# Optimization experiments

Hardware: AMD Instinct MI355X
Metric: run time of the kernel (lower is better)

The kernel has to match this reference:

```python
import jax, jax.numpy as jnp
import numpy as np

MAX_CHILD = 64  # max trie branching factor (padding width for per-row child windows)


def setup_inputs() -> dict:
    key = jax.random.key(0)
    B, D, V, N = 1024, 1024, 32000, 200000
    k1, k2, k3, k4 = jax.random.split(key, 4)
    x = jax.random.normal(k1, (B, D), dtype=jnp.float32)
    weight = jax.random.normal(k2, (V, D), dtype=jnp.float32) * 0.02
    bias = jax.random.normal(k3, (V,), dtype=jnp.float32) * 0.02
    # Build a consistent CompactCSRTrie: offsets [N+1], tokens/child_nodes [E]
    rng = np.random.default_rng(0)
    deg = rng.integers(1, MAX_CHILD + 1, size=N)
    offsets = np.zeros(N + 1, dtype=np.int32)
    offsets[1:] = np.cumsum(deg)
    E = int(offsets[-1])
    tokens = rng.integers(0, V, size=E).astype(np.int32)
    child_nodes = rng.integers(0, N, size=E).astype(np.int32)
    cur_node = jax.random.randint(k4, (B,), 0, N, dtype=jnp.int32)
    return {
        "x": x,
        "weight": weight,
        "bias": bias,
        "cur_node": cur_node,
        "offsets": jnp.asarray(offsets),
        "tokens": jnp.asarray(tokens),
        "child_nodes": jnp.asarray(child_nodes),
        "step": 1,
    }


def reference(x, weight, bias, cur_node, offsets, tokens, child_nodes, step):
    # Dense GEMM part of the fused kernel: logits = x @ W^T + b  -> [B, V]
    logits = jnp.einsum("bd,vd->bv", x, weight) + bias
    B, V = logits.shape

    # CSR trie traversal: per row, the children of cur_node are
    # tokens[offsets[cur]:offsets[cur+1]] (valid next tokens) and
    # child_nodes[...] (next trie nodes). Gather a padded MAX_CHILD window.
    start = offsets[cur_node]                              # [B]
    deg = offsets[cur_node + 1] - start                    # [B]
    pos = jnp.arange(MAX_CHILD, dtype=start.dtype)         # [C]
    idx = jnp.minimum(start[:, None] + pos[None, :], tokens.shape[0] - 1)  # [B, C]
    valid = pos[None, :] < deg[:, None]                    # [B, C] bool

    tok = tokens[idx]                                      # [B, C] valid token columns
    child = child_nodes[idx]                               # [B, C] next trie nodes

    # Validity masking: only valid child tokens keep their logit, rest -> -inf
    rows = jnp.arange(B)[:, None]
    mask = jnp.zeros((B, V), dtype=bool).at[rows, tok].max(valid)
    masked_logits = jnp.where(mask, logits, -jnp.inf)

    next_nodes = jnp.where(valid, child, -1)               # [B, C], -1 padded
    valid_idxs = jnp.where(valid, tok, -1)                 # [B, C], -1 padded
    return next_nodes, valid_idxs, masked_logits
```

## Files before the change

kernel.cpp:

```cpp
#include <hip/hip_runtime.h>
#include <math.h>

#define B_ 1024
#define D_ 1024
#define V_ 32000
#define MAXC 64
#define BLOCK 1024

#define NEG_FILL (-3.0e38f)

typedef float vfloat4 __attribute__((ext_vector_type(4)));

__global__ __launch_bounds__(BLOCK) void constrained_linear_kernel(
    const float* __restrict__ x,
    const float* __restrict__ weight,
    const float* __restrict__ bias,
    const int* __restrict__ cur_node,
    const int* __restrict__ offsets,
    const int* __restrict__ tokens,
    const int* __restrict__ child_nodes,
    float* __restrict__ next_nodes,
    float* __restrict__ valid_idxs,
    float* __restrict__ masked_logits)
{
    __shared__ float xs[D_];
    const int b = blockIdx.x;
    const int tid = threadIdx.x;

    const float4* x4 = reinterpret_cast<const float4*>(x + (size_t)b * D_);
    float4* xs4 = reinterpret_cast<float4*>(xs);
    if (tid < D_ / 4) xs4[tid] = x4[tid];

    const int cur = cur_node[b];
    const int start = offsets[cur];
    int deg = offsets[cur + 1] - start;
    if (deg > MAXC) deg = MAXC;

    float* ml_row = masked_logits + (size_t)b * V_;
    vfloat4* ml4 = reinterpret_cast<vfloat4*>(ml_row);
    const vfloat4 fill4 = {NEG_FILL, NEG_FILL, NEG_FILL, NEG_FILL};
    #pragma unroll 2
    for (int i = tid; i < V_ / 4; i += BLOCK)
        __builtin_nontemporal_store(fill4, &ml4[i]);

    if (tid < MAXC) {
        float nn = -1.0f, vi = -1.0f;
        if (tid < deg) {
            const int e = start + tid;
            nn = (float)child_nodes[e];
            vi = (float)tokens[e];
        }
        next_nodes[b * MAXC + tid] = nn;
        valid_idxs[b * MAXC + tid] = vi;
    }

    __syncthreads();

    const int wave = tid >> 6;
    const int lane = tid & 63;

    for (int c = wave; c < deg; c += BLOCK / 64) {
        const int tok = tokens[start + c];
        const float4* w4 = reinterpret_cast<const float4*>(weight + (size_t)tok * D_);
        float acc = 0.0f;
        #pragma unroll
        for (int k = 0; k < 4; ++k) {
            const float4 wv = w4[k * 64 + lane];
            const float4 xv = xs4[k * 64 + lane];
            acc += wv.x * xv.x + wv.y * xv.y + wv.z * xv.z + wv.w * xv.w;
        }
        #pragma unroll
        for (int off = 32; off > 0; off >>= 1)
            acc += __shfl_xor(acc, off);
        if (lane == 0)
            __builtin_nontemporal_store(acc + bias[tok], &ml_row[tok]);
    }
}

extern "C" void kernel_launch(void* const* d_in, const int* in_sizes, int n_in,
                              void* d_out, int out_size, void* d_ws, size_t ws_size,
                              hipStream_t stream) {
    const float* x           = (const float*)d_in[0];
    const float* weight      = (const float*)d_in[1];
    const float* bias        = (const float*)d_in[2];
    const int*   cur_node    = (const int*)d_in[3];
    const int*   offsets     = (const int*)d_in[4];
    const int*   tokens      = (const int*)d_in[5];
    const int*   child_nodes = (const int*)d_in[6];

    float* out = (float*)d_out;
    float* next_nodes    = out;
    float* valid_idxs    = out + (size_t)B_ * MAXC;
    float* masked_logits = out + 2 * (size_t)B_ * MAXC;

    constrained_linear_kernel<<<B_, BLOCK, 0, stream>>>(
        x, weight, bias, cur_node, offsets, tokens, child_nodes,
        next_nodes, valid_idxs, masked_logits);
}
```

Baseline: 48.93 us.

## Split into separate fill kernel and per-child wave-parallel gather kernel

Replaces the single per-row kernel with two launches. A grid-stride fill kernel writes the -1 padding and the -inf sentinel over the whole output, and a gather kernel gives each (row, child) pair its own wave to compute the dot product and scatter the logit. This removes the per-row barrier and the uneven work across rows, and spreads the 131 MB fill over a flat grid. In exchange it adds a second launch, rewrites the padded slots twice, and reads x from global memory instead of shared memory.

Measured after the change: 63.90 us. 1.31x slower.

```diff
diff --git a/kernel.cpp b/kernel.cpp
--- a/kernel.cpp
+++ b/kernel.cpp
@@ -5,13 +5,30 @@
 #define D_ 1024
 #define V_ 32000
 #define MAXC 64
-#define BLOCK 1024
 
 #define NEG_FILL (-3.0e38f)
 
 typedef float vfloat4 __attribute__((ext_vector_type(4)));
 
-__global__ __launch_bounds__(BLOCK) void constrained_linear_kernel(
+#define FILL_BLOCKS 2048
+#define FILL_TPB 256
+#define NV4 ((2 * B_ * MAXC) / 4)
+#define TOT4 ((2 * B_ * MAXC + B_ * V_) / 4)
+
+__global__ __launch_bounds__(FILL_TPB) void fill_kernel(float* __restrict__ out)
+{
+    vfloat4* o4 = reinterpret_cast<vfloat4*>(out);
+    const vfloat4 neg1 = {-1.0f, -1.0f, -1.0f, -1.0f};
+    const vfloat4 sent = {NEG_FILL, NEG_FILL, NEG_FILL, NEG_FILL};
+    for (int i = blockIdx.x * FILL_TPB + threadIdx.x; i < TOT4;
+         i += FILL_BLOCKS * FILL_TPB) {
+        __builtin_nontemporal_store(i < NV4 ? neg1 : sent, &o4[i]);
+    }
+}
+
+#define G_TPB 1024
+
+__global__ __launch_bounds__(G_TPB) void gather_kernel(
     const float* __restrict__ x,
     const float* __restrict__ weight,
     const float* __restrict__ bias,
@@ -23,58 +40,37 @@
     float* __restrict__ valid_idxs,
     float* __restrict__ masked_logits)
 {
-    __shared__ float xs[D_];
-    const int b = blockIdx.x;
-    const int tid = threadIdx.x;
-
-    const float4* x4 = reinterpret_cast<const float4*>(x + (size_t)b * D_);
-    float4* xs4 = reinterpret_cast<float4*>(xs);
-    if (tid < D_ / 4) xs4[tid] = x4[tid];
+    const int gw = blockIdx.x * (G_TPB / 64) + (threadIdx.x >> 6);
+    const int lane = threadIdx.x & 63;
+    const int b = gw >> 6;
+    const int c = gw & (MAXC - 1);
 
     const int cur = cur_node[b];
     const int start = offsets[cur];
-    int deg = offsets[cur + 1] - start;
-    if (deg > MAXC) deg = MAXC;
+    const int deg = offsets[cur + 1] - start;
+    if (c >= deg) return;
 
-    float* ml_row = masked_logits + (size_t)b * V_;
-    vfloat4* ml4 = reinterpret_cast<vfloat4*>(ml_row);
-    const vfloat4 fill4 = {NEG_FILL, NEG_FILL, NEG_FILL, NEG_FILL};
-    #pragma unroll 2
-    for (int i = tid; i < V_ / 4; i += BLOCK)
-        __builtin_nontemporal_store(fill4, &ml4[i]);
+    const int e = start + c;
+    const int tok = tokens[e];
 
-    if (tid < MAXC) {
-        float nn = -1.0f, vi = -1.0f;
-        if (tid < deg) {
-            const int e = start + tid;
-            nn = (float)child_nodes[e];
-            vi = (float)tokens[e];
-        }
-        next_nodes[b * MAXC + tid] = nn;
-        valid_idxs[b * MAXC + tid] = vi;
+    if (lane == 0) valid_idxs[b * MAXC + c] = (float)tok;
+    if (lane == 1) next_nodes[b * MAXC + c] = (float)child_nodes[e];
+
+    const float4* w4 = reinterpret_cast<const float4*>(weight + (size_t)tok * D_);
+    const float4* x4 = reinterpret_cast<const float4*>(x + (size_t)b * D_);
+    float acc = 0.0f;
+    #pragma unroll
+    for (int k = 0; k < 4; ++k) {
+        const float4 wv = w4[k * 64 + lane];
+        const float4 xv = x4[k * 64 + lane];
+        acc += wv.x * xv.x + wv.y * xv.y + wv.z * xv.z + wv.w * xv.w;
     }
+    #pragma unroll
+    for (int off = 32; off > 0; off >>= 1)
+        acc += __shfl_xor(acc, off);
 
-    __syncthreads();
-
-    const int wave = tid >> 6;
-    const int lane = tid & 63;
-
-    for (int c = wave; c < deg; c += BLOCK / 64) {
-        const int tok = tokens[start + c];
-        const float4* w4 = reinterpret_cast<const float4*>(weight + (size_t)tok * D_);
-        float acc = 0.0f;
-        #pragma unroll
-        for (int k = 0; k < 4; ++k) {
-            const float4 wv = w4[k * 64 + lane];
-            const float4 xv = xs4[k * 64 + lane];
-            acc += wv.x * xv.x + wv.y * xv.y + wv.z * xv.z + wv.w * xv.w;
-        }
-        #pragma unroll
-        for (int off = 32; off > 0; off >>= 1)
-            acc += __shfl_xor(acc, off);
-        if (lane == 0)
-            __builtin_nontemporal_store(acc + bias[tok], &ml_row[tok]);
-    }
+    if (lane == 0)
+        masked_logits[(size_t)b * V_ + tok] = acc + bias[tok];
 }
 
 extern "C" void kernel_launch(void* const* d_in, const int* in_sizes, int n_in,
@@ -93,7 +89,8 @@
     float* valid_idxs    = out + (size_t)B_ * MAXC;
     float* masked_logits = out + 2 * (size_t)B_ * MAXC;
 
-    constrained_linear_kernel<<<B_, BLOCK, 0, stream>>>(
+    fill_kernel<<<FILL_BLOCKS, FILL_TPB, 0, stream>>>(out);
+    gather_kernel<<<(B_ * MAXC) / (G_TPB / 64), G_TPB, 0, stream>>>(
         x, weight, bias, cur_node, offsets, tokens, child_nodes,
         next_nodes, valid_idxs, masked_logits);
 }
```

## Prefetch weight rows into registers before fill stores and drop shared x staging

Applied to the files above, without the earlier changes.

Each wave now loads its x slice and all of its up-to-four assigned weight rows into registers before the fill loop, so the gather latency overlaps the -inf fill stores of the logit row. The dot products are computed before the barrier, and only the final scalar writes happen after it. Shared memory staging of x is removed, and launch bounds request 4 waves per SIMD. The cost is much higher register pressure (64 float4 weight values per lane), which may cap occupancy or cause spills.

Result: faster. 47.73 us (-2.5%).

```diff
diff --git a/kernel.cpp b/kernel.cpp
--- a/kernel.cpp
+++ b/kernel.cpp
@@ -11,7 +11,7 @@
 
 typedef float vfloat4 __attribute__((ext_vector_type(4)));
 
-__global__ __launch_bounds__(BLOCK) void constrained_linear_kernel(
+__global__ __launch_bounds__(BLOCK, 4) void constrained_linear_kernel(
     const float* __restrict__ x,
     const float* __restrict__ weight,
     const float* __restrict__ bias,
@@ -23,25 +23,39 @@
     float* __restrict__ valid_idxs,
     float* __restrict__ masked_logits)
 {
-    __shared__ float xs[D_];
     const int b = blockIdx.x;
     const int tid = threadIdx.x;
-
-    const float4* x4 = reinterpret_cast<const float4*>(x + (size_t)b * D_);
-    float4* xs4 = reinterpret_cast<float4*>(xs);
-    if (tid < D_ / 4) xs4[tid] = x4[tid];
+    const int wave = tid >> 6;
+    const int lane = tid & 63;
 
     const int cur = cur_node[b];
     const int start = offsets[cur];
     int deg = offsets[cur + 1] - start;
     if (deg > MAXC) deg = MAXC;
 
-    float* ml_row = masked_logits + (size_t)b * V_;
-    vfloat4* ml4 = reinterpret_cast<vfloat4*>(ml_row);
-    const vfloat4 fill4 = {NEG_FILL, NEG_FILL, NEG_FILL, NEG_FILL};
-    #pragma unroll 2
-    for (int i = tid; i < V_ / 4; i += BLOCK)
-        __builtin_nontemporal_store(fill4, &ml4[i]);
+    const float4* x4 = reinterpret_cast<const float4*>(x + (size_t)b * D_);
+    float4 xv[4];
+    #pragma unroll
+    for (int k = 0; k < 4; ++k)
+        xv[k] = x4[k * 64 + lane];
+
+    float4 wv[4][4];
+    float bj[4];
+    int   tk[4];
+    #pragma unroll
+    for (int j = 0; j < 4; ++j) {
+        const int c = wave + 16 * j;
+        if (c < deg) {
+            const int e = start + c;
+            const int t = tokens[e];
+            tk[j] = t;
+            bj[j] = bias[t];
+            const float4* w4 = reinterpret_cast<const float4*>(weight + (size_t)t * D_);
+            #pragma unroll
+            for (int k = 0; k < 4; ++k)
+                wv[j][k] = w4[k * 64 + lane];
+        }
+    }
 
     if (tid < MAXC) {
         float nn = -1.0f, vi = -1.0f;
@@ -54,26 +68,37 @@
         valid_idxs[b * MAXC + tid] = vi;
     }
 
+    float* ml_row = masked_logits + (size_t)b * V_;
+    vfloat4* ml4 = reinterpret_cast<vfloat4*>(ml_row);
+    const vfloat4 sent = {NEG_FILL, NEG_FILL, NEG_FILL, NEG_FILL};
+    #pragma unroll 2
+    for (int i = tid; i < V_ / 4; i += BLOCK)
+        __builtin_nontemporal_store(sent, &ml4[i]);
+
+    float accs[4];
+    #pragma unroll
+    for (int j = 0; j < 4; ++j) {
+        const int c = wave + 16 * j;
+        if (c < deg) {
+            float acc = 0.0f;
+            #pragma unroll
+            for (int k = 0; k < 4; ++k)
+                acc += wv[j][k].x * xv[k].x + wv[j][k].y * xv[k].y +
+                       wv[j][k].z * xv[k].z + wv[j][k].w * xv[k].w;
+            #pragma unroll
+            for (int off = 32; off > 0; off >>= 1)
+                acc += __shfl_xor(acc, off);
+            accs[j] = acc + bj[j];
+        }
+    }
+
     __syncthreads();
 
-    const int wave = tid >> 6;
-    const int lane = tid & 63;
-
-    for (int c = wave; c < deg; c += BLOCK / 64) {
-        const int tok = tokens[start + c];
-        const float4* w4 = reinterpret_cast<const float4*>(weight + (size_t)tok * D_);
-        float acc = 0.0f;
-        #pragma unroll
-        for (int k = 0; k < 4; ++k) {
-            const float4 wv = w4[k * 64 + lane];
-            const float4 xv = xs4[k * 64 + lane];
-            acc += wv.x * xv.x + wv.y * xv.y + wv.z * xv.z + wv.w * xv.w;
-        }
-        #pragma unroll
-        for (int off = 32; off > 0; off >>= 1)
-            acc += __shfl_xor(acc, off);
-        if (lane == 0)
-            __builtin_nontemporal_store(acc + bias[tok], &ml_row[tok]);
+    #pragma unroll
+    for (int j = 0; j < 4; ++j) {
+        const int c = wave + 16 * j;
+        if (c < deg && lane == 0)
+            ml_row[tk[j]] = accs[j];
     }
 }
 
```

## Split each row across sixteen vocab-slice blocks with slice-local dot products

Applied to the files above, without the earlier changes.

The grid becomes 16 blocks of 256 threads per batch row instead of one 1024-thread block. Each block fills only its 2000-token slice of the masked logits row with the sentinel and computes dot products only for child tokens that fall in that slice. Winning values are staged in shared memory and written after a barrier, which orders them after the fill in the same block and drops the cross-block fill race. x is now read straight from global memory rather than staged in LDS, and a row's dot-product work can pile up in the few slices that hold its tokens.

After: 48.28 us. About the same (-1.3%).

```diff
diff --git a/kernel.cpp b/kernel.cpp
--- a/kernel.cpp
+++ b/kernel.cpp
@@ -5,13 +5,15 @@
 #define D_ 1024
 #define V_ 32000
 #define MAXC 64
-#define BLOCK 1024
+#define NSLICE 16
+#define SLICE_TOK 2000
+#define SLICE_F4 500
 
 #define NEG_FILL (-3.0e38f)
 
 typedef float vfloat4 __attribute__((ext_vector_type(4)));
 
-__global__ __launch_bounds__(BLOCK) void constrained_linear_kernel(
+__global__ __launch_bounds__(256, 8) void constrained_linear_kernel(
     const float* __restrict__ x,
     const float* __restrict__ weight,
     const float* __restrict__ bias,
@@ -23,57 +25,77 @@
     float* __restrict__ valid_idxs,
     float* __restrict__ masked_logits)
 {
-    __shared__ float xs[D_];
-    const int b = blockIdx.x;
-    const int tid = threadIdx.x;
+    __shared__ int   ltok[MAXC];
+    __shared__ float lval[MAXC];
 
-    const float4* x4 = reinterpret_cast<const float4*>(x + (size_t)b * D_);
-    float4* xs4 = reinterpret_cast<float4*>(xs);
-    if (tid < D_ / 4) xs4[tid] = x4[tid];
+    const int bid  = blockIdx.x;
+    const int b    = bid >> 4;
+    const int q    = bid & (NSLICE - 1);
+    const int tid  = threadIdx.x;
+    const int wave = tid >> 6;
+    const int lane = tid & 63;
 
     const int cur = cur_node[b];
     const int start = offsets[cur];
     int deg = offsets[cur + 1] - start;
     if (deg > MAXC) deg = MAXC;
 
-    float* ml_row = masked_logits + (size_t)b * V_;
-    vfloat4* ml4 = reinterpret_cast<vfloat4*>(ml_row);
-    const vfloat4 fill4 = {NEG_FILL, NEG_FILL, NEG_FILL, NEG_FILL};
-    #pragma unroll 2
-    for (int i = tid; i < V_ / 4; i += BLOCK)
-        __builtin_nontemporal_store(fill4, &ml4[i]);
+    int tok = -1;
+    bool match = false;
+    float bv = 0.0f;
+    const int slot = wave * 16 + (lane & 15);
+    if (lane < 16 && slot < deg) {
+        tok = tokens[start + slot];
+        match = ((unsigned)tok / SLICE_TOK) == (unsigned)q;
+    }
+    if (lane < 16) ltok[wave * 16 + lane] = match ? tok : -1;
+    if (match) bv = bias[tok];
+    unsigned long long mask = __ballot(match);
 
-    if (tid < MAXC) {
+    if (tid < 4) {
+        const int c = q * 4 + tid;
         float nn = -1.0f, vi = -1.0f;
-        if (tid < deg) {
-            const int e = start + tid;
+        if (c < deg) {
+            const int e = start + c;
             nn = (float)child_nodes[e];
             vi = (float)tokens[e];
         }
-        next_nodes[b * MAXC + tid] = nn;
-        valid_idxs[b * MAXC + tid] = vi;
+        next_nodes[b * MAXC + c] = nn;
+        valid_idxs[b * MAXC + c] = vi;
     }
 
-    __syncthreads();
+    float* ml_row = masked_logits + (size_t)b * V_;
+    vfloat4* ml4 = reinterpret_cast<vfloat4*>(ml_row);
+    const vfloat4 sent = {NEG_FILL, NEG_FILL, NEG_FILL, NEG_FILL};
+    for (int i = q * SLICE_F4 + tid; i < (q + 1) * SLICE_F4; i += 256)
+        __builtin_nontemporal_store(sent, &ml4[i]);
 
-    const int wave = tid >> 6;
-    const int lane = tid & 63;
-
-    for (int c = wave; c < deg; c += BLOCK / 64) {
-        const int tok = tokens[start + c];
-        const float4* w4 = reinterpret_cast<const float4*>(weight + (size_t)tok * D_);
+    const float4* x4 = reinterpret_cast<const float4*>(x + (size_t)b * D_);
+    while (mask) {
+        const int s = __builtin_ctzll(mask);
+        mask &= mask - 1;
+        const int t = __shfl(tok, s);
+        const float4* w4 = reinterpret_cast<const float4*>(weight + (size_t)t * D_);
         float acc = 0.0f;
         #pragma unroll
         for (int k = 0; k < 4; ++k) {
             const float4 wv = w4[k * 64 + lane];
-            const float4 xv = xs4[k * 64 + lane];
+            const float4 xv = x4[k * 64 + lane];
             acc += wv.x * xv.x + wv.y * xv.y + wv.z * xv.z + wv.w * xv.w;
         }
         #pragma unroll
         for (int off = 32; off > 0; off >>= 1)
             acc += __shfl_xor(acc, off);
-        if (lane == 0)
-            __builtin_nontemporal_store(acc + bias[tok], &ml_row[tok]);
+        if (lane == s)
+            lval[wave * 16 + s] = acc + bv;
+    }
+
+    __syncthreads();
+
+    if (tid < MAXC) {
+        const int t = ltok[tid];
+        if (t >= 0)
+            ml_row[t] = lval[tid];
     }
 }
 
@@ -93,7 +115,7 @@
     float* valid_idxs    = out + (size_t)B_ * MAXC;
     float* masked_logits = out + 2 * (size_t)B_ * MAXC;
 
-    constrained_linear_kernel<<<B_, BLOCK, 0, stream>>>(
+    constrained_linear_kernel<<<B_ * NSLICE, 256, 0, stream>>>(
         x, weight, bias, cur_node, offsets, tokens, child_nodes,
         next_nodes, valid_idxs, masked_logits);
 }
```
